# Kernel tuning notes

Measured on AMD Instinct MI355X. Metric: run time of the kernel, lower is better.

## Reference

```python
import jax, jax.numpy as jnp
import numpy as np

D_MODEL = 4096
N_EXPERTS = 64
LN_EPS = 1e-5


def setup_inputs() -> dict:
    key = jax.random.key(0)
    k_x, k_w, k_b = jax.random.split(key, 3)
    x = jax.random.normal(k_x, (4, 4096, D_MODEL), dtype=jnp.float32)
    # LayerNorm affine params (torch defaults: ones / zeros)
    gamma = jnp.ones((D_MODEL,), dtype=jnp.float32)
    beta = jnp.zeros((D_MODEL,), dtype=jnp.float32)
    # Linear(d_model, n): weight (n, d), bias (n) — kaiming-uniform-ish init
    bound = 1.0 / np.sqrt(D_MODEL)
    W = jax.random.uniform(k_w, (N_EXPERTS, D_MODEL), dtype=jnp.float32, minval=-bound, maxval=bound)
    b = jax.random.uniform(k_b, (N_EXPERTS,), dtype=jnp.float32, minval=-bound, maxval=bound)
    return {"x": x, "gamma": gamma, "beta": beta, "W": W, "b": b, "top_k": 2}


def reference(x, gamma, beta, W, b, top_k):
    # LayerNorm over last dim
    mu = jnp.mean(x, axis=-1, keepdims=True)
    var = jnp.mean(jnp.square(x - mu), axis=-1, keepdims=True)
    xn = (x - mu) * jax.lax.rsqrt(var + LN_EPS) * gamma + beta
    # Gate projection: (B,T,d) @ (d,n) -> (B,T,n)
    logits = jnp.einsum('btd,nd->btn', xn, W) + b
    weights = jax.nn.softmax(logits, axis=-1)  # (B,T,n)
    k = min(int(top_k), weights.shape[-1])
    topk_vals, indices = jax.lax.top_k(weights, k)  # (B,T,k)
    # scatter top-k values back to dense (B,T,n), then renormalize
    onehot = jax.nn.one_hot(indices, weights.shape[-1], dtype=weights.dtype)  # (B,T,k,n)
    sparse_w = jnp.einsum('btkn,btk->btn', onehot, topk_vals)
    sparse_w = sparse_w / (jnp.sum(sparse_w, axis=-1, keepdims=True) + 1e-8)
    # load-balance (entropy) loss on dense weights
    mean_w = jnp.mean(weights, axis=(0, 1))  # (n,)
    lb_loss = -jnp.sum(mean_w * jnp.log(mean_w + 1e-8))
    return sparse_w, indices, lb_loss
```

## Files before the change

### kernel.cpp

```cpp
#include <hip/hip_runtime.h>
#include <math.h>

#define D_MODEL 4096
#define N_EXP   64
#define N_ROWS  16384
#define LN_EPS  1e-5f
#define TMB     32
#define NBLK    (N_ROWS / TMB)
#define NSTEP   64

typedef __attribute__((ext_vector_type(4))) float f32x4;
typedef __attribute__((ext_vector_type(8))) short s16x8;

struct U4 { unsigned v[4]; };

__device__ __forceinline__ unsigned pkt(float a, float b) {
  unsigned ua = __builtin_bit_cast(unsigned, a);
  unsigned ub = __builtin_bit_cast(unsigned, b);
  return (ua >> 16) | (ub & 0xffff0000u);
}
__device__ __forceinline__ float lo2f(unsigned p) { return __builtin_bit_cast(float, p << 16); }
__device__ __forceinline__ float hi2f(unsigned p) { return __builtin_bit_cast(float, p & 0xffff0000u); }

__device__ __forceinline__ void split8(const float* f, U4& u1, U4& u2, U4& u3) {
#pragma unroll
  for (int i = 0; i < 4; ++i) {
    const float a = f[2 * i], b = f[2 * i + 1];
    const unsigned p1 = pkt(a, b);
    const float ra = a - lo2f(p1), rb = b - hi2f(p1);
    const unsigned p2 = pkt(ra, rb);
    const float sa = ra - lo2f(p2), sb = rb - hi2f(p2);
    u1.v[i] = p1; u2.v[i] = p2; u3.v[i] = pkt(sa, sb);
  }
}


__global__ __launch_bounds__(64) void prep_bpre(
    const float* __restrict__ W, const float* __restrict__ gamma,
    float* __restrict__ Bpre)
{
  const int b = blockIdx.x;
  const int kb32 = b >> 2, j0 = b & 3;
  const int L = threadIdx.x, q = L >> 4, c = L & 15;
  const int n  = j0 * 16 + c;
  const int k0 = kb32 * 32 + q * 8;
  const float4 w0 = *(const float4*)(W + (size_t)n * D_MODEL + k0);
  const float4 w1 = *(const float4*)(W + (size_t)n * D_MODEL + k0 + 4);
  const float4 g0 = *(const float4*)(gamma + k0);
  const float4 g1 = *(const float4*)(gamma + k0 + 4);
  float f[8] = {w0.x * g0.x, w0.y * g0.y, w0.z * g0.z, w0.w * g0.w,
                w1.x * g1.x, w1.y * g1.y, w1.z * g1.z, w1.w * g1.w};
  U4 u1, u2, u3;
  split8(f, u1, u2, u3);
  const size_t base = ((size_t)kb32 * 12 + j0 * 3) * 64 + L;
  *(float4*)(Bpre + (base + 0 * 64) * 4) = __builtin_bit_cast(float4, u1);
  *(float4*)(Bpre + (base + 1 * 64) * 4) = __builtin_bit_cast(float4, u2);
  *(float4*)(Bpre + (base + 2 * 64) * 4) = __builtin_bit_cast(float4, u3);
}

__global__ __launch_bounds__(256) void prep_gc(
    const float* __restrict__ W, const float* __restrict__ gamma,
    const float* __restrict__ beta, const float* __restrict__ bias,
    float* __restrict__ G, float* __restrict__ C)
{
  const int e = blockIdx.x, t = threadIdx.x;
  float sg = 0.f, sb = 0.f;
#pragma unroll
  for (int i = 0; i < 4; ++i) {
    const int d = (i * 256 + t) * 4;
    const float4 wv = *(const float4*)(W + (size_t)e * D_MODEL + d);
    const float4 gv = *(const float4*)(gamma + d);
    const float4 bv = *(const float4*)(beta + d);
    sg += wv.x * gv.x + wv.y * gv.y + wv.z * gv.z + wv.w * gv.w;
    sb += wv.x * bv.x + wv.y * bv.y + wv.z * bv.z + wv.w * bv.w;
  }
#pragma unroll
  for (int o = 32; o > 0; o >>= 1) {
    sg += __shfl_xor(sg, o, 64);
    sb += __shfl_xor(sb, o, 64);
  }
  __shared__ float rg_[4], rb_[4];
  const int wid = t >> 6, ln = t & 63;
  if (ln == 0) { rg_[wid] = sg; rb_[wid] = sb; }
  __syncthreads();
  if (t == 0) {
    G[e] = rg_[0] + rg_[1] + rg_[2] + rg_[3];
    C[e] = rb_[0] + rb_[1] + rb_[2] + rb_[3] + bias[e];
  }
}

__device__ __forceinline__ void gload_lds16(const float* g, const float4* l) {
  __builtin_amdgcn_global_load_lds(
      (const __attribute__((address_space(1))) void*)(g),
      (__attribute__((address_space(3))) void*)(l),
      16, 0, 0);
}

__device__ __forceinline__ void stage24(const float* __restrict__ Bpre,
                                        float4* dst, int nk, int w, int L)
{
  const float* src = Bpre + (((size_t)nk * 24 + w * 6) * 64 + L) * 4;
  float4* d = dst + (size_t)(w * 6) * 64;
#pragma unroll
  for (int i = 0; i < 6; ++i)
    gload_lds16(src + (size_t)i * 256, d + (size_t)i * 64);
}

__device__ __forceinline__ void loadA32(const float* aptr, int j, int ks, float4 A[2]) {
  const float* ap = aptr + (size_t)(j * 2 + ks) * 32;
  A[0] = *(const float4*)(ap);
  A[1] = *(const float4*)(ap + 4);
}

__device__ __forceinline__ void compute_step(
    const float4* __restrict__ buf, int ks, int L,
    const float4 A[2], f32x4 acc[4], float& Sp, float& Qp)
{
  const int PA[6] = {0, 0, 1, 0, 1, 2};
  const int PB[6] = {0, 1, 0, 2, 1, 0};
  s16x8 bf[4][3];
#pragma unroll
  for (int j0 = 0; j0 < 4; ++j0)
#pragma unroll
    for (int tt = 0; tt < 3; ++tt)
      bf[j0][tt] = __builtin_bit_cast(s16x8, buf[(size_t)(ks * 12 + j0 * 3 + tt) * 64 + L]);
  const float4 a0 = A[0], a1 = A[1];
  const float f[8] = {a0.x, a0.y, a0.z, a0.w, a1.x, a1.y, a1.z, a1.w};
#pragma unroll
  for (int i = 0; i < 8; ++i) { Sp += f[i]; Qp = fmaf(f[i], f[i], Qp); }
  U4 u1, u2, u3;
  split8(f, u1, u2, u3);
  const s16x8 af[3] = {__builtin_bit_cast(s16x8, u1),
                       __builtin_bit_cast(s16x8, u2),
                       __builtin_bit_cast(s16x8, u3)};
#pragma unroll
  for (int p = 0; p < 6; ++p)
#pragma unroll
    for (int j0 = 0; j0 < 4; ++j0)
      acc[j0] = __builtin_amdgcn_mfma_f32_16x16x32_bf16(af[PA[p]], bf[j0][PB[p]],
                                                        acc[j0], 0, 0, 0);
}

__global__ __launch_bounds__(256, 2) void router_main(
    const float* __restrict__ x, const float* __restrict__ Bpre,
    const float* __restrict__ G, const float* __restrict__ C,
    float* __restrict__ out_sw, float* __restrict__ out_idx,
    float* __restrict__ out_partials, int k)
{
  const int t = threadIdx.x, w = t >> 6, L = t & 63;
  const int q = L >> 4, c = L & 15;
  const int g = w & 1;
  const int ks = w >> 1;
  const int blk = blockIdx.x;
  const int row0 = blk * TMB + g * 16;

  const float* aptr = x + (size_t)(row0 + c) * D_MODEL + q * 8;

  union Smem {
    float4 B[2][24 * 64];
    struct { float red[2][64][19]; float sm[2][64]; } ep;
  };
  __shared__ Smem S;

  f32x4 acc[4];
#pragma unroll
  for (int j0 = 0; j0 < 4; ++j0) acc[j0] = (f32x4){0.f, 0.f, 0.f, 0.f};
  float Sp = 0.f, Qp = 0.f;

  float4 A0[2], A1[2];
  loadA32(aptr, 0, ks, A0);
  stage24(Bpre, S.B[0], 0, w, L);
  __syncthreads();

  for (int j = 0; j < NSTEP; j += 2) {
    stage24(Bpre, S.B[1], j + 1, w, L);
    loadA32(aptr, j + 1, ks, A1);
    compute_step(S.B[0], ks, L, A0, acc, Sp, Qp);
    __syncthreads();

    if (j + 2 < NSTEP) stage24(Bpre, S.B[0], j + 2, w, L);
    loadA32(aptr, (j + 2) & (NSTEP - 1), ks, A0);
    compute_step(S.B[1], ks, L, A1, acc, Sp, Qp);
    __syncthreads();
  }

#pragma unroll
  for (int o = 16; o <= 32; o <<= 1) {
    Sp += __shfl_xor(Sp, o, 64);
    Qp += __shfl_xor(Qp, o, 64);
  }

  if (ks == 1) {
    float* dst = &S.ep.red[g][L][0];
#pragma unroll
    for (int j0 = 0; j0 < 4; ++j0)
#pragma unroll
      for (int i = 0; i < 4; ++i) dst[j0 * 4 + i] = acc[j0][i];
    dst[16] = Sp; dst[17] = Qp;
  }
  __syncthreads();

  if (ks == 0) {
    const float* sp_ = &S.ep.red[g][L][0];
#pragma unroll
    for (int j0 = 0; j0 < 4; ++j0)
#pragma unroll
      for (int i = 0; i < 4; ++i) acc[j0][i] += sp_[j0 * 4 + i];
    Sp += sp_[16]; Qp += sp_[17];

    const float mu = Sp * (1.f / D_MODEL);
    const float rs = rsqrtf(Qp * (1.f / D_MODEL) - mu * mu + LN_EPS);

    float Gv[4], Cv[4];
#pragma unroll
    for (int j0 = 0; j0 < 4; ++j0) { Gv[j0] = G[16 * j0 + c]; Cv[j0] = C[16 * j0 + c]; }

    float mw[4] = {0.f, 0.f, 0.f, 0.f};
#pragma unroll
    for (int i = 0; i < 4; ++i) {
      const int rloc = 4 * q + i;
      const int row  = row0 + rloc;
      const float mui = __shfl(mu, rloc, 64);
      const float rsi = __shfl(rs, rloc, 64);
      float l[4];
#pragma unroll
      for (int j0 = 0; j0 < 4; ++j0)
        l[j0] = rsi * (acc[j0][i] - mui * Gv[j0]) + Cv[j0];
      float mx = fmaxf(fmaxf(l[0], l[1]), fmaxf(l[2], l[3]));
#pragma unroll
      for (int o = 1; o < 16; o <<= 1) mx = fmaxf(mx, __shfl_xor(mx, o, 64));
      float p[4], ss = 0.f;
#pragma unroll
      for (int j0 = 0; j0 < 4; ++j0) { p[j0] = __expf(l[j0] - mx); ss += p[j0]; }
#pragma unroll
      for (int o = 1; o < 16; o <<= 1) ss += __shfl_xor(ss, o, 64);
      float wv[4];
#pragma unroll
      for (int j0 = 0; j0 < 4; ++j0) { wv[j0] = p[j0] / ss; mw[j0] += wv[j0]; }

      int ch[4];
      float denom = 0.f;
      for (int kk = 0; kk < k && kk < 4; ++kk) {
        float vb = -1.f; int eb = 1 << 30;
#pragma unroll
        for (int j0 = 0; j0 < 4; ++j0) {
          const int e = 16 * j0 + c;
          bool skip = false;
          for (int z = 0; z < kk; ++z) skip |= (ch[z] == e);
          const float cand = skip ? -1.f : wv[j0];
          if (cand > vb || (cand == vb && e < eb)) { vb = cand; eb = e; }
        }
#pragma unroll
        for (int o = 1; o < 16; o <<= 1) {
          const float ov = __shfl_xor(vb, o, 64);
          const int   oe = __shfl_xor(eb, o, 64);
          if (ov > vb || (ov == vb && oe < eb)) { vb = ov; eb = oe; }
        }
        ch[kk] = eb; denom += vb;
        if (c == 0) out_idx[(size_t)row * k + kk] = (float)eb;
      }
      denom += 1e-8f;
#pragma unroll
      for (int j0 = 0; j0 < 4; ++j0) {
        const int e = 16 * j0 + c;
        bool sel = false;
        for (int z = 0; z < k && z < 4; ++z) sel |= (ch[z] == e);
        out_sw[(size_t)row * N_EXP + e] = sel ? wv[j0] / denom : 0.f;
      }
    }

#pragma unroll
    for (int j0 = 0; j0 < 4; ++j0)
#pragma unroll
      for (int o = 16; o <= 32; o <<= 1) mw[j0] += __shfl_xor(mw[j0], o, 64);
    if (q == 0) {
#pragma unroll
      for (int j0 = 0; j0 < 4; ++j0) S.ep.sm[g][16 * j0 + c] = mw[j0];
    }
  }
  __syncthreads();
  if (t < 64)
    out_partials[blk * 64 + t] = S.ep.sm[0][t] + S.ep.sm[1][t];
}

__global__ __launch_bounds__(256) void loss_kernel(
    const float* __restrict__ partials, float* __restrict__ out_loss)
{
  const int t = threadIdx.x, e = t & 63, qq = t >> 6;
  float s = 0.f;
#pragma unroll 8
  for (int b = 0; b < 128; ++b) s += partials[(qq * 128 + b) * 64 + e];
  __shared__ float sh[256];
  sh[t] = s;
  __syncthreads();
  if (t < 64) {
    const float m = (sh[t] + sh[64 + t] + sh[128 + t] + sh[192 + t]) * (1.f / N_ROWS);
    float v = -m * logf(m + 1e-8f);
#pragma unroll
    for (int o = 32; o > 0; o >>= 1) v += __shfl_xor(v, o, 64);
    if (t == 0) out_loss[0] = v;
  }
}

extern "C" void kernel_launch(void* const* d_in, const int* in_sizes, int n_in,
                              void* d_out, int out_size, void* d_ws, size_t ws_size,
                              hipStream_t stream)
{
  const float* x     = (const float*)d_in[0];
  const float* gamma = (const float*)d_in[1];
  const float* beta  = (const float*)d_in[2];
  const float* W     = (const float*)d_in[3];
  const float* bias  = (const float*)d_in[4];

  float* ws       = (float*)d_ws;
  float* Bpre     = ws;
  float* G        = ws + 393216;
  float* C        = ws + 393280;
  float* partials = ws + 393344;

  int k = (out_size - N_ROWS * N_EXP - 1) / N_ROWS;
  if (k < 1) k = 1;
  if (k > 4) k = 4;

  float* out      = (float*)d_out;
  float* out_sw   = out;
  float* out_idx  = out + (size_t)N_ROWS * N_EXP;
  float* out_loss = out + (size_t)N_ROWS * N_EXP + (size_t)N_ROWS * k;

  hipLaunchKernelGGL(prep_bpre, dim3(512), dim3(64), 0, stream, W, gamma, Bpre);
  hipLaunchKernelGGL(prep_gc, dim3(N_EXP), dim3(256), 0, stream, W, gamma, beta, bias, G, C);
  hipLaunchKernelGGL(router_main, dim3(NBLK), dim3(256), 0, stream,
                     x, Bpre, G, C, out_sw, out_idx, partials, k);
  hipLaunchKernelGGL(loss_kernel, dim3(1), dim3(256), 0, stream, partials, out_loss);
}
```

Before: 424.0 us.

## Double row tile per block and triple-buffer weight staging with one barrier per step

Each block now covers 64 rows with 512 threads (4 row groups × 2 K-splits) instead of 32 rows with 256 threads. This halves how often each block re-reads the preprocessed gate weights relative to the rows it processes, and it spreads the weight staging across 8 waves. The main loop moves from a double buffer with two full syncs per pair of steps to a three-deep LDS ring. Each step uses a manual vmcnt wait plus a single s_barrier, so the next tile's global→LDS loads overlap compute. In exchange it uses more LDS per block and depends on hand-counted vmcnt values, and the last steps issue redundant wrap-around loads; the partial-sum reduction and the loss kernel are adjusted to the halved block count.

```diff
diff --git a/kernel.cpp b/kernel.cpp
--- a/kernel.cpp
+++ b/kernel.cpp
@@ -5,7 +5,7 @@
 #define N_EXP   64
 #define N_ROWS  16384
 #define LN_EPS  1e-5f
-#define TMB     32
+#define TMB     64
 #define NBLK    (N_ROWS / TMB)
 #define NSTEP   64
 
@@ -96,18 +96,18 @@
       16, 0, 0);
 }
 
-__device__ __forceinline__ void stage24(const float* __restrict__ Bpre,
-                                        float4* dst, int nk, int w, int L)
-{
-  const float* src = Bpre + (((size_t)nk * 24 + w * 6) * 64 + L) * 4;
-  float4* d = dst + (size_t)(w * 6) * 64;
-#pragma unroll
-  for (int i = 0; i < 6; ++i)
+__device__ __forceinline__ void stage3(const float* __restrict__ Bpre,
+                                       float4* dst, int nk, int w, int L)
+{
+  const float* src = Bpre + (((size_t)nk * 24 + w * 3) * 64 + L) * 4;
+  float4* d = dst + (size_t)(w * 3) * 64;
+#pragma unroll
+  for (int i = 0; i < 3; ++i)
     gload_lds16(src + (size_t)i * 256, d + (size_t)i * 64);
 }
 
-__device__ __forceinline__ void loadA32(const float* aptr, int j, int ks, float4 A[2]) {
-  const float* ap = aptr + (size_t)(j * 2 + ks) * 32;
+__device__ __forceinline__ void loadA32(const float* aptr, int nk, int ks, float4 A[2]) {
+  const float* ap = aptr + (size_t)(nk * 2 + ks) * 32;
   A[0] = *(const float4*)(ap);
   A[1] = *(const float4*)(ap + 4);
 }
@@ -141,7 +141,7 @@
                                                         acc[j0], 0, 0, 0);
 }
 
-__global__ __launch_bounds__(256, 2) void router_main(
+__global__ __launch_bounds__(512, 2) void router_main(
     const float* __restrict__ x, const float* __restrict__ Bpre,
     const float* __restrict__ G, const float* __restrict__ C,
     float* __restrict__ out_sw, float* __restrict__ out_idx,
@@ -149,16 +149,16 @@
 {
   const int t = threadIdx.x, w = t >> 6, L = t & 63;
   const int q = L >> 4, c = L & 15;
-  const int g = w & 1;
-  const int ks = w >> 1;
+  const int g = w & 3;
+  const int ks = w >> 2;
   const int blk = blockIdx.x;
   const int row0 = blk * TMB + g * 16;
 
   const float* aptr = x + (size_t)(row0 + c) * D_MODEL + q * 8;
 
   union Smem {
-    float4 B[2][24 * 64];
-    struct { float red[2][64][19]; float sm[2][64]; } ep;
+    float4 B[3][24 * 64];
+    struct { float red[4][64][19]; float sm[4][64]; } ep;
   };
   __shared__ Smem S;
 
@@ -168,21 +168,33 @@
   float Sp = 0.f, Qp = 0.f;
 
   float4 A0[2], A1[2];
+
+  stage3(Bpre, &S.B[0][0], 0, w, L);
   loadA32(aptr, 0, ks, A0);
-  stage24(Bpre, S.B[0], 0, w, L);
-  __syncthreads();
-
+  stage3(Bpre, &S.B[1][0], 1, w, L);
+
+#define STEP_BODY(J, BC, AC, AN)                                          \
+  {                                                                       \
+    asm volatile("s_waitcnt vmcnt(5)" ::: "memory");                      \
+    __builtin_amdgcn_s_barrier();                                         \
+    asm volatile("" ::: "memory");                                        \
+    __builtin_amdgcn_sched_barrier(0);                                    \
+    const int bs_ = (BC) ? (BC) - 1 : 2;                 \
+    stage3(Bpre, &S.B[bs_][0], ((J) + 2) & (NSTEP - 1), w, L);            \
+    loadA32(aptr, ((J) + 1) & (NSTEP - 1), ks, AN);                       \
+    compute_step(&S.B[BC][0], ks, L, AC, acc, Sp, Qp);                    \
+  }
+
+  int bc = 0;
   for (int j = 0; j < NSTEP; j += 2) {
-    stage24(Bpre, S.B[1], j + 1, w, L);
-    loadA32(aptr, j + 1, ks, A1);
-    compute_step(S.B[0], ks, L, A0, acc, Sp, Qp);
-    __syncthreads();
-
-    if (j + 2 < NSTEP) stage24(Bpre, S.B[0], j + 2, w, L);
-    loadA32(aptr, (j + 2) & (NSTEP - 1), ks, A0);
-    compute_step(S.B[1], ks, L, A1, acc, Sp, Qp);
-    __syncthreads();
-  }
+    STEP_BODY(j,     bc, A0, A1);
+    bc = (bc == 2) ? 0 : bc + 1;
+    STEP_BODY(j + 1, bc, A1, A0);
+    bc = (bc == 2) ? 0 : bc + 1;
+  }
+#undef STEP_BODY
+
+  __syncthreads();
 
 #pragma unroll
   for (int o = 16; o <= 32; o <<= 1) {
@@ -280,7 +292,7 @@
   }
   __syncthreads();
   if (t < 64)
-    out_partials[blk * 64 + t] = S.ep.sm[0][t] + S.ep.sm[1][t];
+    out_partials[blk * 64 + t] = S.ep.sm[0][t] + S.ep.sm[1][t] + S.ep.sm[2][t] + S.ep.sm[3][t];
 }
 
 __global__ __launch_bounds__(256) void loss_kernel(
@@ -289,7 +301,7 @@
   const int t = threadIdx.x, e = t & 63, qq = t >> 6;
   float s = 0.f;
 #pragma unroll 8
-  for (int b = 0; b < 128; ++b) s += partials[(qq * 128 + b) * 64 + e];
+  for (int b = 0; b < 64; ++b) s += partials[(qq * 64 + b) * 64 + e];
   __shared__ float sh[256];
   sh[t] = s;
   __syncthreads();
@@ -329,7 +341,7 @@
 
   hipLaunchKernelGGL(prep_bpre, dim3(512), dim3(64), 0, stream, W, gamma, Bpre);
   hipLaunchKernelGGL(prep_gc, dim3(N_EXP), dim3(256), 0, stream, W, gamma, beta, bias, G, C);
-  hipLaunchKernelGGL(router_main, dim3(NBLK), dim3(256), 0, stream,
+  hipLaunchKernelGGL(router_main, dim3(NBLK), dim3(512), 0, stream,
                      x, Bpre, G, C, out_sw, out_idx, partials, k);
   hipLaunchKernelGGL(loss_kernel, dim3(1), dim3(256), 0, stream, partials, out_loss);
 }
```

Measured after the change: 417.9 us. No clear change (-1.4%).
